# Performance work log

Hardware: AMD Instinct MI355X
Metric: run time of the kernel (lower is better)

Reference implementation:

```python
import jax, jax.numpy as jnp
import numpy as np

H, D, BETA = 12, 64, 1.0
EPS = 1e-8


def setup_inputs() -> dict:
    key = jax.random.key(0)
    k1, k2 = jax.random.split(key)
    n, dim = 1024, H * D
    x = jax.random.normal(k1, (n, dim), dtype=jnp.float32)
    mask = jnp.ones((n, n), dtype=bool)
    W_qk = jax.random.normal(k2, (2 * H * D, dim), dtype=jnp.float32) / np.sqrt(dim).astype(np.float32)
    return {"x": x, "mask": mask, "W_qk": W_qk}


def _free_energy_heads(xh, mask, W_qk):
    # xh: (H, n, D) unit-norm token vectors per head -> per-head free energy (H,)
    n = xh.shape[1]
    xf = jnp.transpose(xh, (1, 0, 2)).reshape(n, H * D)      # 'h n d -> n (h d)'
    qk = xf @ W_qk.T                                          # (n, 2*H*D), Linear no-bias
    q, k = jnp.split(qk, 2, axis=-1)
    q = jnp.transpose(q.reshape(n, H, D), (1, 0, 2))          # (H, n, D)
    k = jnp.transpose(k.reshape(n, H, D), (1, 0, 2))
    sim = jnp.einsum('hid,hjd->hij', q, k)                    # (H, n, n)
    sim = jnp.where(mask, sim, jnp.finfo(sim.dtype).min)
    J = jax.scipy.special.logsumexp(sim, axis=-1)             # (H, n)
    # t* = root of quadratic: beta*t^2 + (-0.5 - 2 beta J) t + (beta J^2 + 0.5 J - 0.25 beta |x|^2)
    hn = jnp.sum(xh * xh, axis=-1)                            # (H, n), |x_i|^2
    b = -0.5 - 2.0 * BETA * J
    c = BETA * J ** 2 + 0.5 * J - 0.25 * BETA * hn
    t = (-b + jnp.sqrt(b * b - 4.0 * BETA * c)) / (2.0 * BETA)
    v = t - J                                                 # (H, n)
    inv_v = 1.0 / jnp.clip(v, EPS, jnp.finfo(v.dtype).max)    # safe_reciprocal
    phi = (BETA * jnp.sum(t, axis=-1)
           - 0.5 * jnp.sum(jnp.log(v + EPS), axis=-1)
           + 0.25 * BETA * jnp.sum(hn * inv_v, axis=-1))      # (H,)
    log_Z = -0.5 * n * (1.0 + jnp.log(2.0 * BETA)) + phi
    return -log_Z / BETA                                      # (H,)


def reference(x, mask, W_qk):
    n = x.shape[0]
    xh = jnp.transpose(x.reshape(n, H, D), (1, 0, 2))         # (H, n, D)
    xh = xh / jnp.linalg.norm(xh, axis=-1, keepdims=True)
    jac = jax.jacrev(lambda xs: _free_energy_heads(xs, mask, W_qk))(xh)  # (H, H, n, D)
    diag = jnp.diagonal(jac)                                  # (n, D, H): dF_h/dx_h only
    out = jnp.transpose(diag, (0, 2, 1)).reshape(n, H * D)    # 'n d h -> n (h d)'
    return -out
```

## Files before the change

kernel.cpp:

```cpp
#include <hip/hip_runtime.h>
#include <cstdint>

#define NTOK 1024
#define NH   12
#define HD   64
#define DIM  768
#define QKD  1536

static constexpr float C2G = 0.61803398874989485f;

typedef __bf16 bf16x8 __attribute__((ext_vector_type(8)));
typedef __bf16 bf16x4 __attribute__((ext_vector_type(4)));
typedef float  f32x4  __attribute__((ext_vector_type(4)));

#define MFMA16(a, b, c) __builtin_amdgcn_mfma_f32_16x16x32_bf16((a), (b), (c), 0, 0, 0)

#define FRAG(S, outer, ks) (*(const bf16x8*)&S[(outer) + (l & 15)][(ks) * 32 + (l >> 4) * 8])

__global__ __launch_bounds__(256) void prep_k(const float* __restrict__ x,
                                              const float* __restrict__ W,
                                              float* __restrict__ xf,
                                              __bf16* __restrict__ xhb,
                                              __bf16* __restrict__ Wb,
                                              __bf16* __restrict__ WT,
                                              float* __restrict__ Zg) {
  __shared__ float Ws[64][65];
  int b = blockIdx.x, t = threadIdx.x;
  if (b < 3072) {
    int gid  = b * 4 + (t >> 6);
    int lane = t & 63;
    int i = gid / NH, h = gid - i * NH;
    size_t idx = (size_t)i * DIM + h * HD + lane;
    float v = x[idx];
    float ss = v * v;
#pragma unroll
    for (int m = 1; m < 64; m <<= 1) ss += __shfl_xor(ss, m);
    float r = v * rsqrtf(ss);
    xf[idx] = r;
    xhb[idx] = (__bf16)r;
  } else if (b < 4224) {
    int tg = (b - 3072) * 256 + t;
    float4 v = ((const float4*)W)[tg];
    bf16x4 o;
    o[0] = (__bf16)v.x; o[1] = (__bf16)v.y; o[2] = (__bf16)v.z; o[3] = (__bf16)v.w;
    *(bf16x4*)(Wb + (size_t)tg * 4) = o;
  } else if (b < 4248) {
    int bb = b - 4224;
    int h = bb % NH, p = bb / NH;
    int rowbase = p * DIM + h * HD;
#pragma unroll
    for (int rr = 0; rr < 16; ++rr) {
      int row = rr * 4 + (t >> 6), col = t & 63;
      Ws[row][col] = W[(size_t)(rowbase + row) * DIM + h * HD + col];
    }
    __syncthreads();
    __bf16* dst = WT + ((size_t)p * NH + h) * HD * HD;
#pragma unroll
    for (int rr = 0; rr < 16; ++rr) {
      int dlt = rr * 4 + (t >> 6), d = t & 63;
      dst[dlt * HD + d] = (__bf16)Ws[d][dlt];
    }
  } else {
    int zz = b - 4248;
    float4 z4 = make_float4(0.f, 0.f, 0.f, 0.f);
    ((float4*)Zg)[zz * 256 + t] = z4;
  }
}

__global__ __launch_bounds__(256) void gemm_dual_k(const __bf16* __restrict__ A,
                                                   const __bf16* __restrict__ Bt,
                                                   __bf16* __restrict__ qkb,
                                                   __bf16* __restrict__ qkT) {
  __shared__ __align__(16) __bf16 As[2][64][72], Bs[2][64][72];
  int m0 = blockIdx.x * 64, n0 = blockIdx.y * 64;
  int t = threadIdx.x, l = t & 63, w = t >> 6;
  int R = (w >> 1) * 32, Cc = (w & 1) * 32;
  int srow = t >> 2, scol = (t & 3) * 16;
  uint4 aA = *(const uint4*)(A  + (size_t)(m0 + srow) * DIM + scol);
  uint4 aB = *(const uint4*)(A  + (size_t)(m0 + srow) * DIM + scol + 8);
  uint4 bA = *(const uint4*)(Bt + (size_t)(n0 + srow) * DIM + scol);
  uint4 bB = *(const uint4*)(Bt + (size_t)(n0 + srow) * DIM + scol + 8);
  f32x4 acc[2][2] = {};
  for (int kt = 0; kt < 12; ++kt) {
    int buf = kt & 1;
    *(uint4*)&As[buf][srow][scol]     = aA;
    *(uint4*)&As[buf][srow][scol + 8] = aB;
    *(uint4*)&Bs[buf][srow][scol]     = bA;
    *(uint4*)&Bs[buf][srow][scol + 8] = bB;
    if (kt < 11) {
      int k0 = (kt + 1) * 64;
      aA = *(const uint4*)(A  + (size_t)(m0 + srow) * DIM + k0 + scol);
      aB = *(const uint4*)(A  + (size_t)(m0 + srow) * DIM + k0 + scol + 8);
      bA = *(const uint4*)(Bt + (size_t)(n0 + srow) * DIM + k0 + scol);
      bB = *(const uint4*)(Bt + (size_t)(n0 + srow) * DIM + k0 + scol + 8);
    }
    __syncthreads();
#pragma unroll
    for (int ks = 0; ks < 2; ++ks) {
      bf16x8 af[2], bf[2];
#pragma unroll
      for (int mf = 0; mf < 2; ++mf) af[mf] = FRAG(As[buf], R + mf * 16, ks);
#pragma unroll
      for (int nf = 0; nf < 2; ++nf) bf[nf] = FRAG(Bs[buf], Cc + nf * 16, ks);
#pragma unroll
      for (int mf = 0; mf < 2; ++mf)
#pragma unroll
        for (int nf = 0; nf < 2; ++nf) acc[mf][nf] = MFMA16(af[mf], bf[nf], acc[mf][nf]);
    }
  }
#pragma unroll
  for (int mf = 0; mf < 2; ++mf)
#pragma unroll
    for (int nf = 0; nf < 2; ++nf) {
      int rowb = m0 + R + mf * 16 + (l >> 4) * 4;
      int col  = n0 + Cc + nf * 16 + (l & 15);
      bf16x4 o4;
#pragma unroll
      for (int r = 0; r < 4; ++r) {
        __bf16 v = (__bf16)acc[mf][nf][r];
        o4[r] = v;
        qkb[(size_t)(rowb + r) * QKD + col] = v;
      }
      *(bf16x4*)(qkT + (size_t)col * NTOK + rowb) = o4;
    }
}

__global__ __launch_bounds__(256) void kbarp_k(const __bf16* __restrict__ qkb,
                                               const __bf16* __restrict__ qkT,
                                               float* __restrict__ part_k,
                                               float* __restrict__ Zg) {
  __shared__ __align__(16) __bf16 Qs[64][72], Ks[2][64][72], KTs[2][64][72], Es[64][72];
  int u = blockIdx.x;
  int h = u >> 5, rem = u & 31;
  int i0 = (rem >> 1) * 64;
  int jt0 = (rem & 1) * 8;
  int t = threadIdx.x, l = t & 63, w = t >> 6;
  int R = (w >> 1) * 32, Cc = (w & 1) * 32;
  int srow = t >> 2, scol = (t & 3) * 16;
  const __bf16* kbase  = qkb + DIM + h * HD;
  const __bf16* ktbase = qkT + (size_t)(DIM + h * HD + srow) * NTOK;
  *(uint4*)&Qs[srow][scol]     = *(const uint4*)(qkb + (size_t)(i0 + srow) * QKD + h * HD + scol);
  *(uint4*)&Qs[srow][scol + 8] = *(const uint4*)(qkb + (size_t)(i0 + srow) * QKD + h * HD + scol + 8);
  uint4 kA = *(const uint4*)(kbase + (size_t)(jt0 * 64 + srow) * QKD + scol);
  uint4 kB = *(const uint4*)(kbase + (size_t)(jt0 * 64 + srow) * QKD + scol + 8);
  uint4 tA = *(const uint4*)(ktbase + jt0 * 64 + scol);
  uint4 tB = *(const uint4*)(ktbase + jt0 * 64 + scol + 8);
  f32x4 facc[2][2] = {};
  float zacc[8] = {0.f, 0.f, 0.f, 0.f, 0.f, 0.f, 0.f, 0.f};
  for (int jt = jt0; jt < jt0 + 8; ++jt) {
    int buf = jt & 1;
    *(uint4*)&Ks[buf][srow][scol]      = kA;
    *(uint4*)&Ks[buf][srow][scol + 8]  = kB;
    *(uint4*)&KTs[buf][srow][scol]     = tA;
    *(uint4*)&KTs[buf][srow][scol + 8] = tB;
    if (jt < jt0 + 7) {
      int j0 = (jt + 1) * 64;
      kA = *(const uint4*)(kbase + (size_t)(j0 + srow) * QKD + scol);
      kB = *(const uint4*)(kbase + (size_t)(j0 + srow) * QKD + scol + 8);
      tA = *(const uint4*)(ktbase + j0 + scol);
      tB = *(const uint4*)(ktbase + j0 + scol + 8);
    }
    __syncthreads();
    f32x4 sacc[2][2] = {};
#pragma unroll
    for (int ks = 0; ks < 2; ++ks) {
      bf16x8 af[2], bf[2];
#pragma unroll
      for (int mf = 0; mf < 2; ++mf) af[mf] = FRAG(Qs, R + mf * 16, ks);
#pragma unroll
      for (int nf = 0; nf < 2; ++nf) bf[nf] = FRAG(Ks[buf], Cc + nf * 16, ks);
#pragma unroll
      for (int mf = 0; mf < 2; ++mf)
#pragma unroll
        for (int nf = 0; nf < 2; ++nf) sacc[mf][nf] = MFMA16(af[mf], bf[nf], sacc[mf][nf]);
    }
#pragma unroll
    for (int mf = 0; mf < 2; ++mf)
#pragma unroll
      for (int r = 0; r < 4; ++r) {
        float e0 = __expf(sacc[mf][0][r]);
        float e1 = __expf(sacc[mf][1][r]);
        zacc[mf * 4 + r] += e0 + e1;
        int row = R + mf * 16 + (l >> 4) * 4 + r;
        Es[row][Cc + (l & 15)]      = (__bf16)e0;
        Es[row][Cc + 16 + (l & 15)] = (__bf16)e1;
      }
    __syncthreads();
#pragma unroll
    for (int ks = 0; ks < 2; ++ks) {
      bf16x8 af[2], bf[2];
#pragma unroll
      for (int mf = 0; mf < 2; ++mf) af[mf] = FRAG(Es, R + mf * 16, ks);
#pragma unroll
      for (int nf = 0; nf < 2; ++nf) bf[nf] = FRAG(KTs[buf], Cc + nf * 16, ks);
#pragma unroll
      for (int mf = 0; mf < 2; ++mf)
#pragma unroll
        for (int nf = 0; nf < 2; ++nf) facc[mf][nf] = MFMA16(af[mf], bf[nf], facc[mf][nf]);
    }
  }
  float* pk = part_k + (size_t)u * 4096;
#pragma unroll
  for (int mf = 0; mf < 2; ++mf)
#pragma unroll
    for (int nf = 0; nf < 2; ++nf)
#pragma unroll
      for (int r = 0; r < 4; ++r) {
        int row = R + mf * 16 + (l >> 4) * 4 + r;
        int col = Cc + nf * 16 + (l & 15);
        pk[row * 64 + col] = facc[mf][nf][r];
      }
#pragma unroll
  for (int zi = 0; zi < 8; ++zi) {
    float z = zacc[zi];
    z += __shfl_xor(z, 1); z += __shfl_xor(z, 2);
    z += __shfl_xor(z, 4); z += __shfl_xor(z, 8);
    if ((l & 15) == 0) {
      int row = R + (zi >> 2) * 16 + (l >> 4) * 4 + (zi & 3);
      atomicAdd(&Zg[(size_t)h * NTOK + i0 + row], z);
    }
  }
}

__global__ __launch_bounds__(256) void qbarp_k(const __bf16* __restrict__ qkb,
                                               const __bf16* __restrict__ qkT,
                                               const float* __restrict__ Zg,
                                               float* __restrict__ part_q) {
  __shared__ __align__(16) __bf16 Ks[64][72], Qs[2][64][72], QTs[2][64][72], Es[64][72];
  int u = blockIdx.x;
  int h = u >> 5, rem = u & 31;
  int j0 = (rem >> 1) * 64;
  int it0 = (rem & 1) * 8;
  int t = threadIdx.x, l = t & 63, w = t >> 6;
  int R = (w >> 1) * 32, Cc = (w & 1) * 32;
  int srow = t >> 2, scol = (t & 3) * 16;
  const __bf16* qbase  = qkb + h * HD;
  const __bf16* qtbase = qkT + (size_t)(h * HD + srow) * NTOK;
  const float*  zb     = Zg + (size_t)h * NTOK;
  *(uint4*)&Ks[srow][scol]     = *(const uint4*)(qkb + (size_t)(j0 + srow) * QKD + DIM + h * HD + scol);
  *(uint4*)&Ks[srow][scol + 8] = *(const uint4*)(qkb + (size_t)(j0 + srow) * QKD + DIM + h * HD + scol + 8);
  uint4 qA = *(const uint4*)(qbase + (size_t)(it0 * 64 + srow) * QKD + scol);
  uint4 qB = *(const uint4*)(qbase + (size_t)(it0 * 64 + srow) * QKD + scol + 8);
  uint4 tA = *(const uint4*)(qtbase + it0 * 64 + scol);
  uint4 tB = *(const uint4*)(qtbase + it0 * 64 + scol + 8);
  f32x4 facc[2][2] = {};
  for (int it = it0; it < it0 + 8; ++it) {
    int buf = it & 1;
    *(uint4*)&Qs[buf][srow][scol]      = qA;
    *(uint4*)&Qs[buf][srow][scol + 8]  = qB;
    *(uint4*)&QTs[buf][srow][scol]     = tA;
    *(uint4*)&QTs[buf][srow][scol + 8] = tB;
    if (it < it0 + 7) {
      int i0 = (it + 1) * 64;
      qA = *(const uint4*)(qbase + (size_t)(i0 + srow) * QKD + scol);
      qB = *(const uint4*)(qbase + (size_t)(i0 + srow) * QKD + scol + 8);
      tA = *(const uint4*)(qtbase + i0 + scol);
      tB = *(const uint4*)(qtbase + i0 + scol + 8);
    }
    __syncthreads();
    f32x4 sacc[2][2] = {};
#pragma unroll
    for (int ks = 0; ks < 2; ++ks) {
      bf16x8 af[2], bf[2];
#pragma unroll
      for (int mf = 0; mf < 2; ++mf) af[mf] = FRAG(Ks, R + mf * 16, ks);
#pragma unroll
      for (int nf = 0; nf < 2; ++nf) bf[nf] = FRAG(Qs[buf], Cc + nf * 16, ks);
#pragma unroll
      for (int mf = 0; mf < 2; ++mf)
#pragma unroll
        for (int nf = 0; nf < 2; ++nf) sacc[mf][nf] = MFMA16(af[mf], bf[nf], sacc[mf][nf]);
    }
    float iz0 = 1.0f / zb[it * 64 + Cc + (l & 15)];
    float iz1 = 1.0f / zb[it * 64 + Cc + 16 + (l & 15)];
#pragma unroll
    for (int mf = 0; mf < 2; ++mf)
#pragma unroll
      for (int r = 0; r < 4; ++r) {
        float e0 = __expf(sacc[mf][0][r]) * iz0;
        float e1 = __expf(sacc[mf][1][r]) * iz1;
        int row = R + mf * 16 + (l >> 4) * 4 + r;
        Es[row][Cc + (l & 15)]      = (__bf16)e0;
        Es[row][Cc + 16 + (l & 15)] = (__bf16)e1;
      }
    __syncthreads();
#pragma unroll
    for (int ks = 0; ks < 2; ++ks) {
      bf16x8 af[2], bf[2];
#pragma unroll
      for (int mf = 0; mf < 2; ++mf) af[mf] = FRAG(Es, R + mf * 16, ks);
#pragma unroll
      for (int nf = 0; nf < 2; ++nf) bf[nf] = FRAG(QTs[buf], Cc + nf * 16, ks);
#pragma unroll
      for (int mf = 0; mf < 2; ++mf)
#pragma unroll
        for (int nf = 0; nf < 2; ++nf) facc[mf][nf] = MFMA16(af[mf], bf[nf], facc[mf][nf]);
    }
  }
  float* pq = part_q + (size_t)u * 4096;
#pragma unroll
  for (int mf = 0; mf < 2; ++mf)
#pragma unroll
    for (int nf = 0; nf < 2; ++nf)
#pragma unroll
      for (int r = 0; r < 4; ++r) {
        int row = R + mf * 16 + (l >> 4) * 4 + r;
        int col = Cc + nf * 16 + (l & 15);
        pq[row * 64 + col] = facc[mf][nf][r];
      }
}

__global__ __launch_bounds__(256) void final2_k(const float* __restrict__ part_k,
                                                const float* __restrict__ part_q,
                                                const float* __restrict__ Zg,
                                                const __bf16* __restrict__ WT,
                                                const float* __restrict__ xf,
                                                float* __restrict__ out) {
  __shared__ __align__(16) __bf16 Ka[64][72], Qa[64][72], WqS[64][72], WkS[64][72];
  int u = blockIdx.x;
  int h = u >> 4, jidx = u & 15, j0 = jidx * 64;
  int t = threadIdx.x, l = t & 63, w = t >> 6;
  int R = (w >> 1) * 32, Cc = (w & 1) * 32;
  int srow = t >> 2, scol = (t & 3) * 16;
  const float* pk = part_k + ((size_t)(h * 32 + jidx * 2)) * 4096;
  const float* pq = part_q + ((size_t)(h * 32 + jidx * 2)) * 4096;
#pragma unroll
  for (int mf = 0; mf < 2; ++mf)
#pragma unroll
    for (int r = 0; r < 4; ++r) {
      int row = R + mf * 16 + (l >> 4) * 4 + r;
      float iz = 1.0f / Zg[(size_t)h * NTOK + j0 + row];
#pragma unroll
      for (int nf = 0; nf < 2; ++nf) {
        int col = Cc + nf * 16 + (l & 15);
        int off = row * 64 + col;
        Ka[row][col] = (__bf16)((pk[off] + pk[4096 + off]) * iz);
        Qa[row][col] = (__bf16)(pq[off] + pq[4096 + off]);
      }
    }
  const __bf16* wq = WT + (size_t)h * HD * HD;
  const __bf16* wk = WT + ((size_t)NH + h) * HD * HD;
  *(uint4*)&WqS[srow][scol]     = *(const uint4*)(wq + (size_t)srow * HD + scol);
  *(uint4*)&WqS[srow][scol + 8] = *(const uint4*)(wq + (size_t)srow * HD + scol + 8);
  *(uint4*)&WkS[srow][scol]     = *(const uint4*)(wk + (size_t)srow * HD + scol);
  *(uint4*)&WkS[srow][scol + 8] = *(const uint4*)(wk + (size_t)srow * HD + scol + 8);
  __syncthreads();
  f32x4 acc[2][2] = {};
#pragma unroll
  for (int ks = 0; ks < 2; ++ks) {
    bf16x8 af[2], bf[2];
#pragma unroll
    for (int mf = 0; mf < 2; ++mf) af[mf] = FRAG(Ka, R + mf * 16, ks);
#pragma unroll
    for (int nf = 0; nf < 2; ++nf) bf[nf] = FRAG(WqS, Cc + nf * 16, ks);
#pragma unroll
    for (int mf = 0; mf < 2; ++mf)
#pragma unroll
      for (int nf = 0; nf < 2; ++nf) acc[mf][nf] = MFMA16(af[mf], bf[nf], acc[mf][nf]);
  }
#pragma unroll
  for (int ks = 0; ks < 2; ++ks) {
    bf16x8 af[2], bf[2];
#pragma unroll
    for (int mf = 0; mf < 2; ++mf) af[mf] = FRAG(Qa, R + mf * 16, ks);
#pragma unroll
    for (int nf = 0; nf < 2; ++nf) bf[nf] = FRAG(WkS, Cc + nf * 16, ks);
#pragma unroll
    for (int mf = 0; mf < 2; ++mf)
#pragma unroll
      for (int nf = 0; nf < 2; ++nf) acc[mf][nf] = MFMA16(af[mf], bf[nf], acc[mf][nf]);
  }
#pragma unroll
  for (int mf = 0; mf < 2; ++mf)
#pragma unroll
    for (int nf = 0; nf < 2; ++nf)
#pragma unroll
      for (int r = 0; r < 4; ++r) {
        int row = j0 + R + mf * 16 + (l >> 4) * 4 + r;
        int col = h * HD + Cc + nf * 16 + (l & 15);
        size_t idx = (size_t)row * DIM + col;
        out[idx] = acc[mf][nf][r] + C2G * xf[idx];
      }
}

extern "C" void kernel_launch(void* const* d_in, const int* in_sizes, int n_in,
                              void* d_out, int out_size, void* d_ws, size_t ws_size,
                              hipStream_t stream) {
  const float* x = (const float*)d_in[0];
  const float* W = (const float*)d_in[2];
  float* out = (float*)d_out;

  float* wsf = (float*)d_ws;
  size_t off = 0;
  float* xf     = wsf + off; off += (size_t)NTOK * DIM;
  float* Zg     = wsf + off; off += (size_t)NH * NTOK;
  float* part_k = wsf + off; off += (size_t)384 * 4096;
  float* part_q = wsf + off; off += (size_t)384 * 4096;
  __bf16* wsb = (__bf16*)(wsf + off);
  size_t boff = 0;
  __bf16* xhb = wsb + boff; boff += (size_t)NTOK * DIM;
  __bf16* Wb  = wsb + boff; boff += (size_t)QKD * DIM;
  __bf16* WT  = wsb + boff; boff += (size_t)2 * NH * HD * HD;
  __bf16* qkb = wsb + boff; boff += (size_t)NTOK * QKD;
  __bf16* qkT = wsb + boff; boff += (size_t)QKD * NTOK;

  prep_k<<<dim3(4260), dim3(256), 0, stream>>>(x, W, xf, xhb, Wb, WT, Zg);
  gemm_dual_k<<<dim3(16, 24), dim3(256), 0, stream>>>(xhb, Wb, qkb, qkT);
  kbarp_k<<<dim3(384), dim3(256), 0, stream>>>(qkb, qkT, part_k, Zg);
  qbarp_k<<<dim3(384), dim3(256), 0, stream>>>(qkb, qkT, Zg, part_q);
  final2_k<<<dim3(192), dim3(256), 0, stream>>>(part_k, part_q, Zg, WT, xf, out);
}
```

Measured before the change: 50.53 us.

## Fuse five-kernel pipeline into one cooperative kernel with grid syncs

```diff
diff --git a/kernel.cpp b/kernel.cpp
--- a/kernel.cpp
+++ b/kernel.cpp
@@ -1,5 +1,8 @@
 #include <hip/hip_runtime.h>
+#include <hip/hip_cooperative_groups.h>
 #include <cstdint>
+
+namespace cg = cooperative_groups;
 
 #define NTOK 1024
 #define NH   12
@@ -16,6 +19,357 @@
 #define MFMA16(a, b, c) __builtin_amdgcn_mfma_f32_16x16x32_bf16((a), (b), (c), 0, 0, 0)
 
 #define FRAG(S, outer, ks) (*(const bf16x8*)&S[(outer) + (l & 15)][(ks) * 32 + (l >> 4) * 8])
+
+__global__ __launch_bounds__(256) void fused_k(
+    const float* __restrict__ x, const float* __restrict__ W,
+    float* __restrict__ xf, __bf16* __restrict__ xhb,
+    __bf16* __restrict__ Wb, __bf16* __restrict__ WT,
+    __bf16* __restrict__ qkb, __bf16* __restrict__ qkT,
+    float* __restrict__ part_k, float* __restrict__ part_q,
+    float* __restrict__ part_z, float* __restrict__ out) {
+  cg::grid_group grid = cg::this_grid();
+  __shared__ __align__(16) __bf16 T[6][64][72];
+  __shared__ float Zs[64];
+  const int b = blockIdx.x, t = threadIdx.x, l = t & 63, w = t >> 6;
+  const int R = (w >> 1) * 32, Cc = (w & 1) * 32;
+  const int srow = t >> 2, scol = (t & 3) * 16;
+
+  {
+#pragma unroll
+    for (int rep = 0; rep < 8; ++rep) {
+      int gid = b * 32 + rep * 4 + w;
+      int i = gid / NH, h = gid - i * NH;
+      size_t idx = (size_t)i * DIM + h * HD + l;
+      float v = x[idx];
+      float ss = v * v;
+#pragma unroll
+      for (int m = 1; m < 64; m <<= 1) ss += __shfl_xor(ss, m);
+      float r = v * rsqrtf(ss);
+      xf[idx] = r;
+      xhb[idx] = (__bf16)r;
+    }
+#pragma unroll
+    for (int rep = 0; rep < 3; ++rep) {
+      int tg = (rep * 384 + b) * 256 + t;
+      float4 v = ((const float4*)W)[tg];
+      bf16x4 o;
+      o[0] = (__bf16)v.x; o[1] = (__bf16)v.y; o[2] = (__bf16)v.z; o[3] = (__bf16)v.w;
+      *(bf16x4*)(Wb + (size_t)tg * 4) = o;
+    }
+    if (b < 24) {
+      float (*Ws)[65] = (float(*)[65])T;
+      int h = b % NH, p = b / NH;
+      int rowbase = p * DIM + h * HD;
+#pragma unroll
+      for (int rr = 0; rr < 16; ++rr) {
+        int row = rr * 4 + (t >> 6), col = t & 63;
+        Ws[row][col] = W[(size_t)(rowbase + row) * DIM + h * HD + col];
+      }
+      __syncthreads();
+      __bf16* dst = WT + ((size_t)p * NH + h) * HD * HD;
+#pragma unroll
+      for (int rr = 0; rr < 16; ++rr) {
+        int dlt = rr * 4 + (t >> 6), d = t & 63;
+        dst[dlt * HD + d] = (__bf16)Ws[d][dlt];
+      }
+    }
+  }
+  __threadfence();
+  grid.sync();
+
+  {
+    int m0 = (b & 15) * 64, n0 = (b >> 4) * 64;
+    uint4 aA = *(const uint4*)(xhb + (size_t)(m0 + srow) * DIM + scol);
+    uint4 aB = *(const uint4*)(xhb + (size_t)(m0 + srow) * DIM + scol + 8);
+    uint4 bA = *(const uint4*)(Wb  + (size_t)(n0 + srow) * DIM + scol);
+    uint4 bB = *(const uint4*)(Wb  + (size_t)(n0 + srow) * DIM + scol + 8);
+    f32x4 acc[2][2] = {};
+    for (int kt = 0; kt < 12; ++kt) {
+      int buf = kt & 1;
+      *(uint4*)&T[buf][srow][scol]         = aA;
+      *(uint4*)&T[buf][srow][scol + 8]     = aB;
+      *(uint4*)&T[2 + buf][srow][scol]     = bA;
+      *(uint4*)&T[2 + buf][srow][scol + 8] = bB;
+      if (kt < 11) {
+        int k0 = (kt + 1) * 64;
+        aA = *(const uint4*)(xhb + (size_t)(m0 + srow) * DIM + k0 + scol);
+        aB = *(const uint4*)(xhb + (size_t)(m0 + srow) * DIM + k0 + scol + 8);
+        bA = *(const uint4*)(Wb  + (size_t)(n0 + srow) * DIM + k0 + scol);
+        bB = *(const uint4*)(Wb  + (size_t)(n0 + srow) * DIM + k0 + scol + 8);
+      }
+      __syncthreads();
+#pragma unroll
+      for (int ks = 0; ks < 2; ++ks) {
+        bf16x8 af[2], bf[2];
+#pragma unroll
+        for (int mf = 0; mf < 2; ++mf) af[mf] = FRAG(T[buf], R + mf * 16, ks);
+#pragma unroll
+        for (int nf = 0; nf < 2; ++nf) bf[nf] = FRAG(T[2 + buf], Cc + nf * 16, ks);
+#pragma unroll
+        for (int mf = 0; mf < 2; ++mf)
+#pragma unroll
+          for (int nf = 0; nf < 2; ++nf) acc[mf][nf] = MFMA16(af[mf], bf[nf], acc[mf][nf]);
+      }
+    }
+#pragma unroll
+    for (int mf = 0; mf < 2; ++mf)
+#pragma unroll
+      for (int nf = 0; nf < 2; ++nf) {
+        int rowb = m0 + R + mf * 16 + (l >> 4) * 4;
+        int col  = n0 + Cc + nf * 16 + (l & 15);
+        bf16x4 o4;
+#pragma unroll
+        for (int r = 0; r < 4; ++r) {
+          __bf16 v = (__bf16)acc[mf][nf][r];
+          o4[r] = v;
+          qkb[(size_t)(rowb + r) * QKD + col] = v;
+        }
+        *(bf16x4*)(qkT + (size_t)col * NTOK + rowb) = o4;
+      }
+  }
+  __threadfence();
+  grid.sync();
+
+  {
+    int h = b >> 5, rem = b & 31;
+    int i0 = (rem >> 1) * 64;
+    int jt0 = (rem & 1) * 8;
+    const __bf16* kbase  = qkb + DIM + h * HD;
+    const __bf16* ktbase = qkT + (size_t)(DIM + h * HD + srow) * NTOK;
+    *(uint4*)&T[0][srow][scol]     = *(const uint4*)(qkb + (size_t)(i0 + srow) * QKD + h * HD + scol);
+    *(uint4*)&T[0][srow][scol + 8] = *(const uint4*)(qkb + (size_t)(i0 + srow) * QKD + h * HD + scol + 8);
+    if (t < 64) Zs[t] = 0.f;
+    uint4 kA = *(const uint4*)(kbase + (size_t)(jt0 * 64 + srow) * QKD + scol);
+    uint4 kB = *(const uint4*)(kbase + (size_t)(jt0 * 64 + srow) * QKD + scol + 8);
+    uint4 tA = *(const uint4*)(ktbase + jt0 * 64 + scol);
+    uint4 tB = *(const uint4*)(ktbase + jt0 * 64 + scol + 8);
+    f32x4 facc[2][2] = {};
+    float zacc[8] = {0.f, 0.f, 0.f, 0.f, 0.f, 0.f, 0.f, 0.f};
+    for (int jt = jt0; jt < jt0 + 8; ++jt) {
+      int buf = jt & 1;
+      *(uint4*)&T[1 + buf][srow][scol]     = kA;
+      *(uint4*)&T[1 + buf][srow][scol + 8] = kB;
+      *(uint4*)&T[3 + buf][srow][scol]     = tA;
+      *(uint4*)&T[3 + buf][srow][scol + 8] = tB;
+      if (jt < jt0 + 7) {
+        int j0 = (jt + 1) * 64;
+        kA = *(const uint4*)(kbase + (size_t)(j0 + srow) * QKD + scol);
+        kB = *(const uint4*)(kbase + (size_t)(j0 + srow) * QKD + scol + 8);
+        tA = *(const uint4*)(ktbase + j0 + scol);
+        tB = *(const uint4*)(ktbase + j0 + scol + 8);
+      }
+      __syncthreads();
+      f32x4 sacc[2][2] = {};
+#pragma unroll
+      for (int ks = 0; ks < 2; ++ks) {
+        bf16x8 af[2], bf[2];
+#pragma unroll
+        for (int mf = 0; mf < 2; ++mf) af[mf] = FRAG(T[0], R + mf * 16, ks);
+#pragma unroll
+        for (int nf = 0; nf < 2; ++nf) bf[nf] = FRAG(T[1 + buf], Cc + nf * 16, ks);
+#pragma unroll
+        for (int mf = 0; mf < 2; ++mf)
+#pragma unroll
+          for (int nf = 0; nf < 2; ++nf) sacc[mf][nf] = MFMA16(af[mf], bf[nf], sacc[mf][nf]);
+      }
+#pragma unroll
+      for (int mf = 0; mf < 2; ++mf)
+#pragma unroll
+        for (int r = 0; r < 4; ++r) {
+          float e0 = __expf(sacc[mf][0][r]);
+          float e1 = __expf(sacc[mf][1][r]);
+          zacc[mf * 4 + r] += e0 + e1;
+          int row = R + mf * 16 + (l >> 4) * 4 + r;
+          T[5][row][Cc + (l & 15)]      = (__bf16)e0;
+          T[5][row][Cc + 16 + (l & 15)] = (__bf16)e1;
+        }
+      __syncthreads();
+#pragma unroll
+      for (int ks = 0; ks < 2; ++ks) {
+        bf16x8 af[2], bf[2];
+#pragma unroll
+        for (int mf = 0; mf < 2; ++mf) af[mf] = FRAG(T[5], R + mf * 16, ks);
+#pragma unroll
+        for (int nf = 0; nf < 2; ++nf) bf[nf] = FRAG(T[3 + buf], Cc + nf * 16, ks);
+#pragma unroll
+        for (int mf = 0; mf < 2; ++mf)
+#pragma unroll
+          for (int nf = 0; nf < 2; ++nf) facc[mf][nf] = MFMA16(af[mf], bf[nf], facc[mf][nf]);
+      }
+    }
+    float* pk = part_k + (size_t)b * 4096;
+#pragma unroll
+    for (int mf = 0; mf < 2; ++mf)
+#pragma unroll
+      for (int nf = 0; nf < 2; ++nf)
+#pragma unroll
+        for (int r = 0; r < 4; ++r) {
+          int row = R + mf * 16 + (l >> 4) * 4 + r;
+          int col = Cc + nf * 16 + (l & 15);
+          pk[row * 64 + col] = facc[mf][nf][r];
+        }
+#pragma unroll
+    for (int zi = 0; zi < 8; ++zi) {
+      float z = zacc[zi];
+      z += __shfl_xor(z, 1); z += __shfl_xor(z, 2);
+      z += __shfl_xor(z, 4); z += __shfl_xor(z, 8);
+      if ((l & 15) == 0) {
+        int row = R + (zi >> 2) * 16 + (l >> 4) * 4 + (zi & 3);
+        atomicAdd(&Zs[row], z);
+      }
+    }
+    __syncthreads();
+    if (t < 64) part_z[(size_t)b * 64 + t] = Zs[t];
+  }
+  __threadfence();
+  grid.sync();
+
+  {
+    int h = b >> 5, rem = b & 31;
+    int j0 = (rem >> 1) * 64;
+    int it0 = (rem & 1) * 8;
+    const __bf16* qbase  = qkb + h * HD;
+    const __bf16* qtbase = qkT + (size_t)(h * HD + srow) * NTOK;
+    const float*  pz     = part_z + (size_t)h * 2048;
+    *(uint4*)&T[0][srow][scol]     = *(const uint4*)(qkb + (size_t)(j0 + srow) * QKD + DIM + h * HD + scol);
+    *(uint4*)&T[0][srow][scol + 8] = *(const uint4*)(qkb + (size_t)(j0 + srow) * QKD + DIM + h * HD + scol + 8);
+    uint4 qA = *(const uint4*)(qbase + (size_t)(it0 * 64 + srow) * QKD + scol);
+    uint4 qB = *(const uint4*)(qbase + (size_t)(it0 * 64 + srow) * QKD + scol + 8);
+    uint4 tA = *(const uint4*)(qtbase + it0 * 64 + scol);
+    uint4 tB = *(const uint4*)(qtbase + it0 * 64 + scol + 8);
+    f32x4 facc[2][2] = {};
+    for (int it = it0; it < it0 + 8; ++it) {
+      int buf = it & 1;
+      *(uint4*)&T[1 + buf][srow][scol]     = qA;
+      *(uint4*)&T[1 + buf][srow][scol + 8] = qB;
+      *(uint4*)&T[3 + buf][srow][scol]     = tA;
+      *(uint4*)&T[3 + buf][srow][scol + 8] = tB;
+      if (it < it0 + 7) {
+        int i0 = (it + 1) * 64;
+        qA = *(const uint4*)(qbase + (size_t)(i0 + srow) * QKD + scol);
+        qB = *(const uint4*)(qbase + (size_t)(i0 + srow) * QKD + scol + 8);
+        tA = *(const uint4*)(qtbase + i0 + scol);
+        tB = *(const uint4*)(qtbase + i0 + scol + 8);
+      }
+      __syncthreads();
+      f32x4 sacc[2][2] = {};
+#pragma unroll
+      for (int ks = 0; ks < 2; ++ks) {
+        bf16x8 af[2], bf[2];
+#pragma unroll
+        for (int mf = 0; mf < 2; ++mf) af[mf] = FRAG(T[0], R + mf * 16, ks);
+#pragma unroll
+        for (int nf = 0; nf < 2; ++nf) bf[nf] = FRAG(T[1 + buf], Cc + nf * 16, ks);
+#pragma unroll
+        for (int mf = 0; mf < 2; ++mf)
+#pragma unroll
+          for (int nf = 0; nf < 2; ++nf) sacc[mf][nf] = MFMA16(af[mf], bf[nf], sacc[mf][nf]);
+      }
+      float iz0 = 1.0f / (pz[it * 128 + Cc + (l & 15)]      + pz[it * 128 + 64 + Cc + (l & 15)]);
+      float iz1 = 1.0f / (pz[it * 128 + Cc + 16 + (l & 15)] + pz[it * 128 + 64 + Cc + 16 + (l & 15)]);
+#pragma unroll
+      for (int mf = 0; mf < 2; ++mf)
+#pragma unroll
+        for (int r = 0; r < 4; ++r) {
+          float e0 = __expf(sacc[mf][0][r]) * iz0;
+          float e1 = __expf(sacc[mf][1][r]) * iz1;
+          int row = R + mf * 16 + (l >> 4) * 4 + r;
+          T[5][row][Cc + (l & 15)]      = (__bf16)e0;
+          T[5][row][Cc + 16 + (l & 15)] = (__bf16)e1;
+        }
+      __syncthreads();
+#pragma unroll
+      for (int ks = 0; ks < 2; ++ks) {
+        bf16x8 af[2], bf[2];
+#pragma unroll
+        for (int mf = 0; mf < 2; ++mf) af[mf] = FRAG(T[5], R + mf * 16, ks);
+#pragma unroll
+        for (int nf = 0; nf < 2; ++nf) bf[nf] = FRAG(T[3 + buf], Cc + nf * 16, ks);
+#pragma unroll
+        for (int mf = 0; mf < 2; ++mf)
+#pragma unroll
+          for (int nf = 0; nf < 2; ++nf) facc[mf][nf] = MFMA16(af[mf], bf[nf], facc[mf][nf]);
+      }
+    }
+    float* pq = part_q + (size_t)b * 4096;
+#pragma unroll
+    for (int mf = 0; mf < 2; ++mf)
+#pragma unroll
+      for (int nf = 0; nf < 2; ++nf)
+#pragma unroll
+        for (int r = 0; r < 4; ++r) {
+          int row = R + mf * 16 + (l >> 4) * 4 + r;
+          int col = Cc + nf * 16 + (l & 15);
+          pq[row * 64 + col] = facc[mf][nf][r];
+        }
+  }
+  __threadfence();
+  grid.sync();
+
+  if (b < 192) {
+    int h = b >> 4, jidx = b & 15, j0 = jidx * 64;
+    const float* pk = part_k + ((size_t)(h * 32 + jidx * 2)) * 4096;
+    const float* pq = part_q + ((size_t)(h * 32 + jidx * 2)) * 4096;
+    const float* pzr = part_z + ((size_t)(h * 32 + jidx * 2)) * 64;
+#pragma unroll
+    for (int mf = 0; mf < 2; ++mf)
+#pragma unroll
+      for (int r = 0; r < 4; ++r) {
+        int row = R + mf * 16 + (l >> 4) * 4 + r;
+        float iz = 1.0f / (pzr[row] + pzr[64 + row]);
+#pragma unroll
+        for (int nf = 0; nf < 2; ++nf) {
+          int col = Cc + nf * 16 + (l & 15);
+          int off = row * 64 + col;
+          T[0][row][col] = (__bf16)((pk[off] + pk[4096 + off]) * iz);
+          T[1][row][col] = (__bf16)(pq[off] + pq[4096 + off]);
+        }
+      }
+    const __bf16* wq = WT + (size_t)h * HD * HD;
+    const __bf16* wk = WT + ((size_t)NH + h) * HD * HD;
+    *(uint4*)&T[2][srow][scol]     = *(const uint4*)(wq + (size_t)srow * HD + scol);
+    *(uint4*)&T[2][srow][scol + 8] = *(const uint4*)(wq + (size_t)srow * HD + scol + 8);
+    *(uint4*)&T[3][srow][scol]     = *(const uint4*)(wk + (size_t)srow * HD + scol);
+    *(uint4*)&T[3][srow][scol + 8] = *(const uint4*)(wk + (size_t)srow * HD + scol + 8);
+    __syncthreads();
+    f32x4 acc[2][2] = {};
+#pragma unroll
+    for (int ks = 0; ks < 2; ++ks) {
+      bf16x8 af[2], bf[2];
+#pragma unroll
+      for (int mf = 0; mf < 2; ++mf) af[mf] = FRAG(T[0], R + mf * 16, ks);
+#pragma unroll
+      for (int nf = 0; nf < 2; ++nf) bf[nf] = FRAG(T[2], Cc + nf * 16, ks);
+#pragma unroll
+      for (int mf = 0; mf < 2; ++mf)
+#pragma unroll
+        for (int nf = 0; nf < 2; ++nf) acc[mf][nf] = MFMA16(af[mf], bf[nf], acc[mf][nf]);
+    }
+#pragma unroll
+    for (int ks = 0; ks < 2; ++ks) {
+      bf16x8 af[2], bf[2];
+#pragma unroll
+      for (int mf = 0; mf < 2; ++mf) af[mf] = FRAG(T[1], R + mf * 16, ks);
+#pragma unroll
+      for (int nf = 0; nf < 2; ++nf) bf[nf] = FRAG(T[3], Cc + nf * 16, ks);
+#pragma unroll
+      for (int mf = 0; mf < 2; ++mf)
+#pragma unroll
+        for (int nf = 0; nf < 2; ++nf) acc[mf][nf] = MFMA16(af[mf], bf[nf], acc[mf][nf]);
+    }
+#pragma unroll
+    for (int mf = 0; mf < 2; ++mf)
+#pragma unroll
+      for (int nf = 0; nf < 2; ++nf)
+#pragma unroll
+        for (int r = 0; r < 4; ++r) {
+          int row = j0 + R + mf * 16 + (l >> 4) * 4 + r;
+          int col = h * HD + Cc + nf * 16 + (l & 15);
+          size_t idx = (size_t)row * DIM + col;
+          out[idx] = acc[mf][nf][r] + C2G * xf[idx];
+        }
+  }
+}
 
 __global__ __launch_bounds__(256) void prep_k(const float* __restrict__ x,
                                               const float* __restrict__ W,
@@ -62,8 +416,7 @@
     }
   } else {
     int zz = b - 4248;
-    float4 z4 = make_float4(0.f, 0.f, 0.f, 0.f);
-    ((float4*)Zg)[zz * 256 + t] = z4;
+    ((float4*)Zg)[zz * 256 + t] = make_float4(0.f, 0.f, 0.f, 0.f);
   }
 }
 
@@ -396,6 +749,7 @@
   float* Zg     = wsf + off; off += (size_t)NH * NTOK;
   float* part_k = wsf + off; off += (size_t)384 * 4096;
   float* part_q = wsf + off; off += (size_t)384 * 4096;
+  float* part_z = wsf + off; off += (size_t)384 * 64;
   __bf16* wsb = (__bf16*)(wsf + off);
   size_t boff = 0;
   __bf16* xhb = wsb + boff; boff += (size_t)NTOK * DIM;
@@ -404,9 +758,23 @@
   __bf16* qkb = wsb + boff; boff += (size_t)NTOK * QKD;
   __bf16* qkT = wsb + boff; boff += (size_t)QKD * NTOK;
 
-  prep_k<<<dim3(4260), dim3(256), 0, stream>>>(x, W, xf, xhb, Wb, WT, Zg);
-  gemm_dual_k<<<dim3(16, 24), dim3(256), 0, stream>>>(xhb, Wb, qkb, qkT);
-  kbarp_k<<<dim3(384), dim3(256), 0, stream>>>(qkb, qkT, part_k, Zg);
-  qbarp_k<<<dim3(384), dim3(256), 0, stream>>>(qkb, qkT, Zg, part_q);
-  final2_k<<<dim3(192), dim3(256), 0, stream>>>(part_k, part_q, Zg, WT, xf, out);
+  int maxb = 0;
+  hipOccupancyMaxActiveBlocksPerMultiprocessor(&maxb, fused_k, 256, 0);
+  int dev = 0, ncu = 0;
+  hipGetDevice(&dev);
+  hipDeviceGetAttribute(&ncu, hipDeviceAttributeMultiprocessorCount, dev);
+  bool coop = (maxb > 0 && ncu > 0 && (long)maxb * ncu >= 384);
+
+  if (coop) {
+    void* args[] = {(void*)&x, (void*)&W, (void*)&xf, (void*)&xhb, (void*)&Wb,
+                    (void*)&WT, (void*)&qkb, (void*)&qkT, (void*)&part_k,
+                    (void*)&part_q, (void*)&part_z, (void*)&out};
+    hipLaunchCooperativeKernel(fused_k, dim3(384), dim3(256), args, 0, stream);
+  } else {
+    prep_k<<<dim3(4260), dim3(256), 0, stream>>>(x, W, xf, xhb, Wb, WT, Zg);
+    gemm_dual_k<<<dim3(16, 24), dim3(256), 0, stream>>>(xhb, Wb, qkb, qkT);
+    kbarp_k<<<dim3(384), dim3(256), 0, stream>>>(qkb, qkT, part_k, Zg);
+    qbarp_k<<<dim3(384), dim3(256), 0, stream>>>(qkb, qkT, Zg, part_q);
+    final2_k<<<dim3(192), dim3(256), 0, stream>>>(part_k, part_q, Zg, WT, xf, out);
+  }
 }
```

Result: no change. 50.27 us (-0.5%).

## Fuse normalization and bf16 conversion into QK projection GEMM, replace global Z atomics

Applied to the files above, without the earlier changes.

```diff
diff --git a/kernel.cpp b/kernel.cpp
--- a/kernel.cpp
+++ b/kernel.cpp
@@ -17,36 +17,24 @@
 
 #define FRAG(S, outer, ks) (*(const bf16x8*)&S[(outer) + (l & 15)][(ks) * 32 + (l >> 4) * 8])
 
-__global__ __launch_bounds__(256) void prep_k(const float* __restrict__ x,
-                                              const float* __restrict__ W,
-                                              float* __restrict__ xf,
-                                              __bf16* __restrict__ xhb,
-                                              __bf16* __restrict__ Wb,
-                                              __bf16* __restrict__ WT,
-                                              float* __restrict__ Zg) {
-  __shared__ float Ws[64][65];
-  int b = blockIdx.x, t = threadIdx.x;
-  if (b < 3072) {
-    int gid  = b * 4 + (t >> 6);
-    int lane = t & 63;
-    int i = gid / NH, h = gid - i * NH;
-    size_t idx = (size_t)i * DIM + h * HD + lane;
-    float v = x[idx];
-    float ss = v * v;
-#pragma unroll
-    for (int m = 1; m < 64; m <<= 1) ss += __shfl_xor(ss, m);
-    float r = v * rsqrtf(ss);
-    xf[idx] = r;
-    xhb[idx] = (__bf16)r;
-  } else if (b < 4224) {
-    int tg = (b - 3072) * 256 + t;
-    float4 v = ((const float4*)W)[tg];
-    bf16x4 o;
-    o[0] = (__bf16)v.x; o[1] = (__bf16)v.y; o[2] = (__bf16)v.z; o[3] = (__bf16)v.w;
-    *(bf16x4*)(Wb + (size_t)tg * 4) = o;
-  } else if (b < 4248) {
-    int bb = b - 4224;
-    int h = bb % NH, p = bb / NH;
+__device__ __forceinline__ bf16x4 cvt4(float4 v, float s) {
+  bf16x4 o;
+  o[0] = (__bf16)(v.x * s); o[1] = (__bf16)(v.y * s);
+  o[2] = (__bf16)(v.z * s); o[3] = (__bf16)(v.w * s);
+  return o;
+}
+
+__global__ __launch_bounds__(256) void prep_gemm_k(
+    const float* __restrict__ x, const float* __restrict__ W,
+    float* __restrict__ xf, __bf16* __restrict__ WT,
+    __bf16* __restrict__ qkb, __bf16* __restrict__ qkT) {
+  __shared__ __align__(16) __bf16 T[4][64][72];
+  const int b = blockIdx.x, t = threadIdx.x, l = t & 63, w = t >> 6;
+  const int srow = t >> 2, scol = (t & 3) * 16;
+
+  if (b < 24) {
+    float (*Ws)[65] = (float(*)[65])T;
+    int h = b % NH, p = b / NH;
     int rowbase = p * DIM + h * HD;
 #pragma unroll
     for (int rr = 0; rr < 16; ++rr) {
@@ -60,76 +48,83 @@
       int dlt = rr * 4 + (t >> 6), d = t & 63;
       dst[dlt * HD + d] = (__bf16)Ws[d][dlt];
     }
-  } else {
-    int zz = b - 4248;
-    float4 z4 = make_float4(0.f, 0.f, 0.f, 0.f);
-    ((float4*)Zg)[zz * 256 + t] = z4;
-  }
-}
-
-__global__ __launch_bounds__(256) void gemm_dual_k(const __bf16* __restrict__ A,
-                                                   const __bf16* __restrict__ Bt,
-                                                   __bf16* __restrict__ qkb,
-                                                   __bf16* __restrict__ qkT) {
-  __shared__ __align__(16) __bf16 As[2][64][72], Bs[2][64][72];
-  int m0 = blockIdx.x * 64, n0 = blockIdx.y * 64;
-  int t = threadIdx.x, l = t & 63, w = t >> 6;
-  int R = (w >> 1) * 32, Cc = (w & 1) * 32;
-  int srow = t >> 2, scol = (t & 3) * 16;
-  uint4 aA = *(const uint4*)(A  + (size_t)(m0 + srow) * DIM + scol);
-  uint4 aB = *(const uint4*)(A  + (size_t)(m0 + srow) * DIM + scol + 8);
-  uint4 bA = *(const uint4*)(Bt + (size_t)(n0 + srow) * DIM + scol);
-  uint4 bB = *(const uint4*)(Bt + (size_t)(n0 + srow) * DIM + scol + 8);
-  f32x4 acc[2][2] = {};
+    __syncthreads();
+  }
+
+  int i0 = (b & 15) * 64, o0 = (b >> 4) * 32;
+  bool wxf = (b >> 4) == 0;
+  int R2 = w * 16;
+  int srow2 = t >> 3, scol2 = (t & 7) * 8;
+  __bf16 (*Bs)[72] = (__bf16(*)[72])&T[2][0][0];
+  const float* xrow = x + (size_t)(i0 + srow) * DIM + scol;
+  const float* wrow = W + (size_t)(o0 + srow2) * DIM + scol2;
+  float4 a4[4], b4[2];
+#pragma unroll
+  for (int q = 0; q < 4; ++q) a4[q] = *(const float4*)(xrow + q * 4);
+#pragma unroll
+  for (int q = 0; q < 2; ++q) b4[q] = *(const float4*)(wrow + q * 4);
+  f32x4 acc[2] = {};
   for (int kt = 0; kt < 12; ++kt) {
     int buf = kt & 1;
-    *(uint4*)&As[buf][srow][scol]     = aA;
-    *(uint4*)&As[buf][srow][scol + 8] = aB;
-    *(uint4*)&Bs[buf][srow][scol]     = bA;
-    *(uint4*)&Bs[buf][srow][scol + 8] = bB;
+    float ss = 0.f;
+#pragma unroll
+    for (int q = 0; q < 4; ++q)
+      ss += a4[q].x * a4[q].x + a4[q].y * a4[q].y + a4[q].z * a4[q].z + a4[q].w * a4[q].w;
+    ss += __shfl_xor(ss, 1);
+    ss += __shfl_xor(ss, 2);
+    float inv = rsqrtf(ss);
+#pragma unroll
+    for (int q = 0; q < 4; ++q) {
+      *(bf16x4*)&T[buf][srow][scol + q * 4] = cvt4(a4[q], inv);
+      if (wxf) {
+        float4 av = make_float4(a4[q].x * inv, a4[q].y * inv, a4[q].z * inv, a4[q].w * inv);
+        *(float4*)(xf + (size_t)(i0 + srow) * DIM + kt * 64 + scol + q * 4) = av;
+      }
+    }
+#pragma unroll
+    for (int q = 0; q < 2; ++q)
+      *(bf16x4*)&Bs[buf * 32 + srow2][scol2 + q * 4] = cvt4(b4[q], 1.0f);
     if (kt < 11) {
-      int k0 = (kt + 1) * 64;
-      aA = *(const uint4*)(A  + (size_t)(m0 + srow) * DIM + k0 + scol);
-      aB = *(const uint4*)(A  + (size_t)(m0 + srow) * DIM + k0 + scol + 8);
-      bA = *(const uint4*)(Bt + (size_t)(n0 + srow) * DIM + k0 + scol);
-      bB = *(const uint4*)(Bt + (size_t)(n0 + srow) * DIM + k0 + scol + 8);
+#pragma unroll
+      for (int q = 0; q < 4; ++q) a4[q] = *(const float4*)(xrow + (kt + 1) * 64 + q * 4);
+#pragma unroll
+      for (int q = 0; q < 2; ++q) b4[q] = *(const float4*)(wrow + (kt + 1) * 64 + q * 4);
     }
     __syncthreads();
 #pragma unroll
     for (int ks = 0; ks < 2; ++ks) {
-      bf16x8 af[2], bf[2];
-#pragma unroll
-      for (int mf = 0; mf < 2; ++mf) af[mf] = FRAG(As[buf], R + mf * 16, ks);
-#pragma unroll
-      for (int nf = 0; nf < 2; ++nf) bf[nf] = FRAG(Bs[buf], Cc + nf * 16, ks);
-#pragma unroll
-      for (int mf = 0; mf < 2; ++mf)
-#pragma unroll
-        for (int nf = 0; nf < 2; ++nf) acc[mf][nf] = MFMA16(af[mf], bf[nf], acc[mf][nf]);
-    }
-  }
-#pragma unroll
-  for (int mf = 0; mf < 2; ++mf)
-#pragma unroll
-    for (int nf = 0; nf < 2; ++nf) {
-      int rowb = m0 + R + mf * 16 + (l >> 4) * 4;
-      int col  = n0 + Cc + nf * 16 + (l & 15);
-      bf16x4 o4;
-#pragma unroll
-      for (int r = 0; r < 4; ++r) {
-        __bf16 v = (__bf16)acc[mf][nf][r];
-        o4[r] = v;
-        qkb[(size_t)(rowb + r) * QKD + col] = v;
-      }
-      *(bf16x4*)(qkT + (size_t)col * NTOK + rowb) = o4;
-    }
+      bf16x8 af = *(const bf16x8*)&T[buf][R2 + (l & 15)][ks * 32 + (l >> 4) * 8];
+#pragma unroll
+      for (int nf = 0; nf < 2; ++nf) {
+        bf16x8 bfr = *(const bf16x8*)&Bs[buf * 32 + nf * 16 + (l & 15)][ks * 32 + (l >> 4) * 8];
+        acc[nf] = MFMA16(af, bfr, acc[nf]);
+      }
+    }
+  }
+  __bf16 (*T4)[40] = (__bf16(*)[40])&T[0][0][0];
+  __bf16 (*T5)[72] = (__bf16(*)[72])&T[3][0][0];
+#pragma unroll
+  for (int nf = 0; nf < 2; ++nf) {
+    bf16x4 p;
+#pragma unroll
+    for (int r = 0; r < 4; ++r) {
+      __bf16 v = (__bf16)acc[nf][r];
+      T4[R2 + (l >> 4) * 4 + r][nf * 16 + (l & 15)] = v;
+      p[r] = v;
+    }
+    *(bf16x4*)&T5[nf * 16 + (l & 15)][R2 + (l >> 4) * 4] = p;
+  }
+  __syncthreads();
+  *(uint4*)(qkb + (size_t)(i0 + (t >> 2)) * QKD + o0 + (t & 3) * 8)  = *(const uint4*)&T4[t >> 2][(t & 3) * 8];
+  *(uint4*)(qkT + (size_t)(o0 + (t >> 3)) * NTOK + i0 + (t & 7) * 8) = *(const uint4*)&T5[t >> 3][(t & 7) * 8];
 }
 
 __global__ __launch_bounds__(256) void kbarp_k(const __bf16* __restrict__ qkb,
                                                const __bf16* __restrict__ qkT,
                                                float* __restrict__ part_k,
-                                               float* __restrict__ Zg) {
+                                               float* __restrict__ part_z) {
   __shared__ __align__(16) __bf16 Qs[64][72], Ks[2][64][72], KTs[2][64][72], Es[64][72];
+  __shared__ float Zs[64];
   int u = blockIdx.x;
   int h = u >> 5, rem = u & 31;
   int i0 = (rem >> 1) * 64;
@@ -141,6 +136,7 @@
   const __bf16* ktbase = qkT + (size_t)(DIM + h * HD + srow) * NTOK;
   *(uint4*)&Qs[srow][scol]     = *(const uint4*)(qkb + (size_t)(i0 + srow) * QKD + h * HD + scol);
   *(uint4*)&Qs[srow][scol + 8] = *(const uint4*)(qkb + (size_t)(i0 + srow) * QKD + h * HD + scol + 8);
+  if (t < 64) Zs[t] = 0.f;
   uint4 kA = *(const uint4*)(kbase + (size_t)(jt0 * 64 + srow) * QKD + scol);
   uint4 kB = *(const uint4*)(kbase + (size_t)(jt0 * 64 + srow) * QKD + scol + 8);
   uint4 tA = *(const uint4*)(ktbase + jt0 * 64 + scol);
@@ -217,14 +213,16 @@
     z += __shfl_xor(z, 4); z += __shfl_xor(z, 8);
     if ((l & 15) == 0) {
       int row = R + (zi >> 2) * 16 + (l >> 4) * 4 + (zi & 3);
-      atomicAdd(&Zg[(size_t)h * NTOK + i0 + row], z);
-    }
-  }
+      atomicAdd(&Zs[row], z);
+    }
+  }
+  __syncthreads();
+  if (t < 64) part_z[(size_t)u * 64 + t] = Zs[t];
 }
 
 __global__ __launch_bounds__(256) void qbarp_k(const __bf16* __restrict__ qkb,
                                                const __bf16* __restrict__ qkT,
-                                               const float* __restrict__ Zg,
+                                               const float* __restrict__ part_z,
                                                float* __restrict__ part_q) {
   __shared__ __align__(16) __bf16 Ks[64][72], Qs[2][64][72], QTs[2][64][72], Es[64][72];
   int u = blockIdx.x;
@@ -236,7 +234,7 @@
   int srow = t >> 2, scol = (t & 3) * 16;
   const __bf16* qbase  = qkb + h * HD;
   const __bf16* qtbase = qkT + (size_t)(h * HD + srow) * NTOK;
-  const float*  zb     = Zg + (size_t)h * NTOK;
+  const float*  pz     = part_z + (size_t)h * 2048;
   *(uint4*)&Ks[srow][scol]     = *(const uint4*)(qkb + (size_t)(j0 + srow) * QKD + DIM + h * HD + scol);
   *(uint4*)&Ks[srow][scol + 8] = *(const uint4*)(qkb + (size_t)(j0 + srow) * QKD + DIM + h * HD + scol + 8);
   uint4 qA = *(const uint4*)(qbase + (size_t)(it0 * 64 + srow) * QKD + scol);
@@ -271,8 +269,8 @@
 #pragma unroll
         for (int nf = 0; nf < 2; ++nf) sacc[mf][nf] = MFMA16(af[mf], bf[nf], sacc[mf][nf]);
     }
-    float iz0 = 1.0f / zb[it * 64 + Cc + (l & 15)];
-    float iz1 = 1.0f / zb[it * 64 + Cc + 16 + (l & 15)];
+    float iz0 = 1.0f / (pz[it * 128 + Cc + (l & 15)]      + pz[it * 128 + 64 + Cc + (l & 15)]);
+    float iz1 = 1.0f / (pz[it * 128 + Cc + 16 + (l & 15)] + pz[it * 128 + 64 + Cc + 16 + (l & 15)]);
 #pragma unroll
     for (int mf = 0; mf < 2; ++mf)
 #pragma unroll
@@ -312,7 +310,7 @@
 
 __global__ __launch_bounds__(256) void final2_k(const float* __restrict__ part_k,
                                                 const float* __restrict__ part_q,
-                                                const float* __restrict__ Zg,
+                                                const float* __restrict__ part_z,
                                                 const __bf16* __restrict__ WT,
                                                 const float* __restrict__ xf,
                                                 float* __restrict__ out) {
@@ -322,14 +320,15 @@
   int t = threadIdx.x, l = t & 63, w = t >> 6;
   int R = (w >> 1) * 32, Cc = (w & 1) * 32;
   int srow = t >> 2, scol = (t & 3) * 16;
-  const float* pk = part_k + ((size_t)(h * 32 + jidx * 2)) * 4096;
-  const float* pq = part_q + ((size_t)(h * 32 + jidx * 2)) * 4096;
+  const float* pk  = part_k + ((size_t)(h * 32 + jidx * 2)) * 4096;
+  const float* pq  = part_q + ((size_t)(h * 32 + jidx * 2)) * 4096;
+  const float* pzr = part_z + ((size_t)(h * 32 + jidx * 2)) * 64;
 #pragma unroll
   for (int mf = 0; mf < 2; ++mf)
 #pragma unroll
     for (int r = 0; r < 4; ++r) {
       int row = R + mf * 16 + (l >> 4) * 4 + r;
-      float iz = 1.0f / Zg[(size_t)h * NTOK + j0 + row];
+      float iz = 1.0f / (pzr[row] + pzr[64 + row]);
 #pragma unroll
       for (int nf = 0; nf < 2; ++nf) {
         int col = Cc + nf * 16 + (l & 15);
@@ -393,20 +392,17 @@
   float* wsf = (float*)d_ws;
   size_t off = 0;
   float* xf     = wsf + off; off += (size_t)NTOK * DIM;
-  float* Zg     = wsf + off; off += (size_t)NH * NTOK;
   float* part_k = wsf + off; off += (size_t)384 * 4096;
   float* part_q = wsf + off; off += (size_t)384 * 4096;
+  float* part_z = wsf + off; off += (size_t)384 * 64;
   __bf16* wsb = (__bf16*)(wsf + off);
   size_t boff = 0;
-  __bf16* xhb = wsb + boff; boff += (size_t)NTOK * DIM;
-  __bf16* Wb  = wsb + boff; boff += (size_t)QKD * DIM;
   __bf16* WT  = wsb + boff; boff += (size_t)2 * NH * HD * HD;
   __bf16* qkb = wsb + boff; boff += (size_t)NTOK * QKD;
   __bf16* qkT = wsb + boff; boff += (size_t)QKD * NTOK;
 
-  prep_k<<<dim3(4260), dim3(256), 0, stream>>>(x, W, xf, xhb, Wb, WT, Zg);
-  gemm_dual_k<<<dim3(16, 24), dim3(256), 0, stream>>>(xhb, Wb, qkb, qkT);
-  kbarp_k<<<dim3(384), dim3(256), 0, stream>>>(qkb, qkT, part_k, Zg);
-  qbarp_k<<<dim3(384), dim3(256), 0, stream>>>(qkb, qkT, Zg, part_q);
-  final2_k<<<dim3(192), dim3(256), 0, stream>>>(part_k, part_q, Zg, WT, xf, out);
-}
+  prep_gemm_k<<<dim3(768), dim3(256), 0, stream>>>(x, W, xf, WT, qkb, qkT);
+  kbarp_k<<<dim3(384), dim3(256), 0, stream>>>(qkb, qkT, part_k, part_z);
+  qbarp_k<<<dim3(384), dim3(256), 0, stream>>>(qkb, qkT, part_z, part_q);
+  final2_k<<<dim3(192), dim3(256), 0, stream>>>(part_k, part_q, part_z, WT, xf, out);
+}
```

Measured after the change: 56.98 us. +12.8%, slower.
